# Performance work log

Measured on AMD Instinct MI355X. Metric: run time of the kernel, lower is better.

## Reference

```python
import jax, jax.numpy as jnp
import numpy as np

A_MIN = 0.001
EPS = 1e-08


def setup_inputs() -> dict:
    key = jax.random.key(0)
    k1, k2, k3, k4 = jax.random.split(key, 4)
    B, O, I = 512, 1024, 512
    x = jax.random.normal(k1, (B, I), dtype=jnp.float32)
    translation = jax.random.uniform(k2, (O, I), dtype=jnp.float32, minval=-1.0, maxval=1.0)
    scale_raw = jax.random.uniform(k3, (O, I), dtype=jnp.float32, minval=-2.0, maxval=0.0)
    weights = jax.random.normal(k4, (O, I), dtype=jnp.float32) * (1.0 / np.sqrt(I))
    return {"x": x, "translation": translation, "scale_raw": scale_raw, "weights": weights}


def reference(x, translation, scale_raw, weights):
    # x: (B, I); params: (O, I)
    scale = A_MIN + jax.nn.softplus(scale_raw)  # (O, I)
    # s: (B, O, I) broadcast intermediate
    s = (x[:, None, :] - translation[None, :, :]) / (scale[None, :, :] + EPS)
    s2 = s * s
    wavelet = (1.0 - s2) * jnp.exp(-0.5 * s2)  # mexican hat
    y = jnp.einsum('oi,boi->bo', weights, wavelet)  # reduce over in_features
    return y
```

## Files before the change

kernel.cpp:

```cpp
#include <hip/hip_runtime.h>
#include <hip/hip_bf16.h>


#define WL_A_MIN 0.001f
#define WL_EPS   1e-8f

constexpr int WL_B = 512;
constexpr int WL_O = 1024;
constexpr int WL_I = 512;

constexpr int O_TILE = 16;
constexpr int B_TILE = 64;
constexpr int KC     = 64;

constexpr int PS = KC * 4 + 4;
constexpr int XS = B_TILE + 4;

#define WL_SQK  0.84932180553704583800f
#define WL_IK   1.38629436111989061883f
#define WL_L2E  1.44269504088896340736f
#define WL_LN2  0.69314718055994530942f

typedef float v2f __attribute__((ext_vector_type(2)));

__device__ __forceinline__ float fast_exp2(float a) {
#if __has_builtin(__builtin_amdgcn_exp2f)
    return __builtin_amdgcn_exp2f(a);
#else
    return exp2f(a);
#endif
}
__device__ __forceinline__ float fast_log2(float a) {
#if __has_builtin(__builtin_amdgcn_logf)
    return __builtin_amdgcn_logf(a);
#else
    return __log2f(a);
#endif
}
__device__ __forceinline__ float fast_rcp(float a) {
#if __has_builtin(__builtin_amdgcn_rcpf)
    return __builtin_amdgcn_rcpf(a);
#else
    return 1.0f / a;
#endif
}

__global__ __launch_bounds__(256, 2) void wl_fused(
    const float* __restrict__ x,
    const float* __restrict__ translation,
    const float* __restrict__ scale_raw,
    const float* __restrict__ weights,
    float* __restrict__ out)
{
    __shared__ float p_lds[O_TILE * PS];
    __shared__ float x_lds[KC * XS];

    const int tid    = threadIdx.x;
    const int ox     = tid & 15;
    const int bg     = tid >> 4;
    const int o_base = blockIdx.x * O_TILE;
    const int b_base = blockIdx.y * B_TILE;

    v2f accA = {0.0f, 0.0f};
    v2f accB = {0.0f, 0.0f};

    for (int kc = 0; kc < WL_I; kc += KC) {
        #pragma unroll
        for (int k = 0; k < 4; ++k) {
            int lin = k * 256 + tid;
            int o_l = lin >> 6;
            int i_l = lin & 63;
            int gi  = (o_base + o_l) * WL_I + kc + i_l;
            float t  = translation[gi];
            float sr = scale_raw[gi];
            float w  = weights[gi];
            float ex    = fast_exp2(sr * WL_L2E);
            float sp    = fast_log2(1.0f + ex) * WL_LN2;
            float inv   = fast_rcp(WL_A_MIN + sp + WL_EPS);
            float inv_s = inv * WL_SQK;
            float4 pv = make_float4(-t * inv_s, inv_s, w, w * WL_IK);
            *reinterpret_cast<float4*>(&p_lds[o_l * PS + i_l * 4]) = pv;
        }
        {
            int b_r = tid & 63;
            int seg = tid >> 6;
            const float* xg = &x[(b_base + b_r) * WL_I + kc + seg * 16];
            #pragma unroll
            for (int q = 0; q < 4; ++q) {
                float4 v = *reinterpret_cast<const float4*>(&xg[q * 4]);
                int i0 = seg * 16 + q * 4;
                x_lds[(i0 + 0) * XS + b_r] = v.x;
                x_lds[(i0 + 1) * XS + b_r] = v.y;
                x_lds[(i0 + 2) * XS + b_r] = v.z;
                x_lds[(i0 + 3) * XS + b_r] = v.w;
            }
        }
        __syncthreads();

        const float* pr = &p_lds[ox * PS];

        #pragma unroll 4
        for (int i = 0; i < KC; ++i) {
            float4 p  = *reinterpret_cast<const float4*>(&pr[i * 4]);
            float4 xq = *reinterpret_cast<const float4*>(&x_lds[i * XS + bg * 4]);
            v2f nti2 = {p.x, p.x};
            v2f inv2 = {p.y, p.y};
            v2f w2   = {p.z, p.z};
            v2f nk2  = {-p.w, -p.w};
            v2f xa = {xq.x, xq.y};
            v2f xb = {xq.z, xq.w};
            v2f sa = __builtin_elementwise_fma(xa, inv2, nti2);
            v2f sb = __builtin_elementwise_fma(xb, inv2, nti2);
            v2f ua = sa * sa;
            v2f ub = sb * sb;
            v2f ea = {fast_exp2(-ua.x), fast_exp2(-ua.y)};
            v2f eb = {fast_exp2(-ub.x), fast_exp2(-ub.y)};
            accA = __builtin_elementwise_fma(w2, ea, accA);
            accB = __builtin_elementwise_fma(w2, eb, accB);
            v2f uea = ua * ea;
            v2f ueb = ub * eb;
            accA = __builtin_elementwise_fma(nk2, uea, accA);
            accB = __builtin_elementwise_fma(nk2, ueb, accB);
        }
        __syncthreads();
    }

    const int o = o_base + ox;
    const int b = b_base + bg * 4;
    out[(b + 0) * WL_O + o] = accA.x;
    out[(b + 1) * WL_O + o] = accA.y;
    out[(b + 2) * WL_O + o] = accB.x;
    out[(b + 3) * WL_O + o] = accB.y;
}

extern "C" void kernel_launch(void* const* d_in, const int* in_sizes, int n_in,
                              void* d_out, int out_size, void* d_ws, size_t ws_size,
                              hipStream_t stream) {
    const float* x           = (const float*)d_in[0];
    const float* translation = (const float*)d_in[1];
    const float* scale_raw   = (const float*)d_in[2];
    const float* weights     = (const float*)d_in[3];
    float*       out         = (float*)d_out;

    wl_fused<<<dim3(WL_O / O_TILE, WL_B / B_TILE), dim3(256), 0, stream>>>(
        x, translation, scale_raw, weights, out);
}
```

Measured before the change: 114.5 us.

## Split parameter preprocessing into separate kernel and stream transposed params from global

Adds a prep kernel that computes the softplus-derived per-(o,i) parameters once and writes them transposed as float4 into workspace. Previously every block in the batch dimension recomputed them. The main kernel stages a 32-row x tile for the full input dimension in LDS and reads the parameters straight from global memory, coalesced across lanes. Each thread now accumulates 8 batch rows instead of 4. This removes redundant transcendental work and the per-chunk syncs, but adds a second launch, an 8 MB workspace round-trip, and one-block-per-CU launch bounds that may reduce latency hiding.

Result: slower. 139.5 us (+21.8%).

```diff
diff --git a/kernel.cpp b/kernel.cpp
--- a/kernel.cpp
+++ b/kernel.cpp
@@ -8,13 +8,6 @@
 constexpr int WL_B = 512;
 constexpr int WL_O = 1024;
 constexpr int WL_I = 512;
-
-constexpr int O_TILE = 16;
-constexpr int B_TILE = 64;
-constexpr int KC     = 64;
-
-constexpr int PS = KC * 4 + 4;
-constexpr int XS = B_TILE + 4;
 
 #define WL_SQK  0.84932180553704583800f
 #define WL_IK   1.38629436111989061883f
@@ -45,92 +38,113 @@
 #endif
 }
 
-__global__ __launch_bounds__(256, 2) void wl_fused(
-    const float* __restrict__ x,
+__global__ __launch_bounds__(256) void wl_prep(
     const float* __restrict__ translation,
     const float* __restrict__ scale_raw,
     const float* __restrict__ weights,
+    float4* __restrict__ pT4)
+{
+    const int lane   = threadIdx.x & 63;
+    const int ic     = threadIdx.x >> 6;
+    const int o      = blockIdx.x * 64 + lane;
+    const int i_base = blockIdx.y * 64 + ic * 16;
+
+    #pragma unroll 4
+    for (int k = 0; k < 16; ++k) {
+        int i  = i_base + k;
+        int gi = o * WL_I + i;
+        float t  = translation[gi];
+        float sr = scale_raw[gi];
+        float w  = weights[gi];
+        float ex    = fast_exp2(sr * WL_L2E);
+        float sp    = fast_log2(1.0f + ex) * WL_LN2;
+        float inv   = fast_rcp(WL_A_MIN + sp + WL_EPS);
+        float inv_s = inv * WL_SQK;
+        pT4[i * WL_O + o] = make_float4(-t * inv_s, inv_s, w, w * WL_IK);
+    }
+}
+
+__global__ __launch_bounds__(256, 1) void wl_main(
+    const float* __restrict__ x,
+    const float4* __restrict__ pT4,
     float* __restrict__ out)
 {
-    __shared__ float p_lds[O_TILE * PS];
-    __shared__ float x_lds[KC * XS];
+    __shared__ float xT[WL_I * 32];
 
-    const int tid    = threadIdx.x;
-    const int ox     = tid & 15;
-    const int bg     = tid >> 4;
-    const int o_base = blockIdx.x * O_TILE;
-    const int b_base = blockIdx.y * B_TILE;
+    const int tid  = threadIdx.x;
+    const int lane = tid & 63;
+    const int wid  = __builtin_amdgcn_readfirstlane(tid >> 6);
+    const int o    = blockIdx.x * 64 + lane;
+    const int b0   = blockIdx.y * 32;
 
-    v2f accA = {0.0f, 0.0f};
-    v2f accB = {0.0f, 0.0f};
+    {
+        const int b_l = tid & 31;
+        const int seg = tid >> 5;
+        const float* xg = &x[(b0 + b_l) * WL_I + seg * 64];
+        #pragma unroll
+        for (int q = 0; q < 16; ++q) {
+            float4 v = *reinterpret_cast<const float4*>(xg + q * 4);
+            int i0 = seg * 64 + q * 4;
+            xT[(i0 + 0) * 32 + b_l] = v.x;
+            xT[(i0 + 1) * 32 + b_l] = v.y;
+            xT[(i0 + 2) * 32 + b_l] = v.z;
+            xT[(i0 + 3) * 32 + b_l] = v.w;
+        }
+    }
+    __syncthreads();
 
-    for (int kc = 0; kc < WL_I; kc += KC) {
-        #pragma unroll
-        for (int k = 0; k < 4; ++k) {
-            int lin = k * 256 + tid;
-            int o_l = lin >> 6;
-            int i_l = lin & 63;
-            int gi  = (o_base + o_l) * WL_I + kc + i_l;
-            float t  = translation[gi];
-            float sr = scale_raw[gi];
-            float w  = weights[gi];
-            float ex    = fast_exp2(sr * WL_L2E);
-            float sp    = fast_log2(1.0f + ex) * WL_LN2;
-            float inv   = fast_rcp(WL_A_MIN + sp + WL_EPS);
-            float inv_s = inv * WL_SQK;
-            float4 pv = make_float4(-t * inv_s, inv_s, w, w * WL_IK);
-            *reinterpret_cast<float4*>(&p_lds[o_l * PS + i_l * 4]) = pv;
-        }
-        {
-            int b_r = tid & 63;
-            int seg = tid >> 6;
-            const float* xg = &x[(b_base + b_r) * WL_I + kc + seg * 16];
-            #pragma unroll
-            for (int q = 0; q < 4; ++q) {
-                float4 v = *reinterpret_cast<const float4*>(&xg[q * 4]);
-                int i0 = seg * 16 + q * 4;
-                x_lds[(i0 + 0) * XS + b_r] = v.x;
-                x_lds[(i0 + 1) * XS + b_r] = v.y;
-                x_lds[(i0 + 2) * XS + b_r] = v.z;
-                x_lds[(i0 + 3) * XS + b_r] = v.w;
-            }
-        }
-        __syncthreads();
+    const float4* pp   = pT4 + o;
+    const float*  xrow = &xT[wid * 8];
 
-        const float* pr = &p_lds[ox * PS];
+    v2f a0 = {0.f, 0.f}, a1 = {0.f, 0.f}, a2 = {0.f, 0.f}, a3 = {0.f, 0.f};
 
-        #pragma unroll 4
-        for (int i = 0; i < KC; ++i) {
-            float4 p  = *reinterpret_cast<const float4*>(&pr[i * 4]);
-            float4 xq = *reinterpret_cast<const float4*>(&x_lds[i * XS + bg * 4]);
-            v2f nti2 = {p.x, p.x};
-            v2f inv2 = {p.y, p.y};
-            v2f w2   = {p.z, p.z};
-            v2f nk2  = {-p.w, -p.w};
-            v2f xa = {xq.x, xq.y};
-            v2f xb = {xq.z, xq.w};
-            v2f sa = __builtin_elementwise_fma(xa, inv2, nti2);
-            v2f sb = __builtin_elementwise_fma(xb, inv2, nti2);
-            v2f ua = sa * sa;
-            v2f ub = sb * sb;
-            v2f ea = {fast_exp2(-ua.x), fast_exp2(-ua.y)};
-            v2f eb = {fast_exp2(-ub.x), fast_exp2(-ub.y)};
-            accA = __builtin_elementwise_fma(w2, ea, accA);
-            accB = __builtin_elementwise_fma(w2, eb, accB);
-            v2f uea = ua * ea;
-            v2f ueb = ub * eb;
-            accA = __builtin_elementwise_fma(nk2, uea, accA);
-            accB = __builtin_elementwise_fma(nk2, ueb, accB);
-        }
-        __syncthreads();
+    #pragma unroll 4
+    for (int i = 0; i < WL_I; ++i) {
+        float4 p = pp[(size_t)i * WL_O];
+        float4 xa = *reinterpret_cast<const float4*>(xrow + i * 32);
+        float4 xb = *reinterpret_cast<const float4*>(xrow + i * 32 + 4);
+
+        v2f nti = {p.x, p.x};
+        v2f inv = {p.y, p.y};
+        v2f w2  = {p.z, p.z};
+        v2f wk  = {p.w, p.w};
+
+        v2f x01 = {xa.x, xa.y};
+        v2f x23 = {xa.z, xa.w};
+        v2f x45 = {xb.x, xb.y};
+        v2f x67 = {xb.z, xb.w};
+
+        v2f s0 = __builtin_elementwise_fma(x01, inv, nti);
+        v2f s1 = __builtin_elementwise_fma(x23, inv, nti);
+        v2f s2 = __builtin_elementwise_fma(x45, inv, nti);
+        v2f s3 = __builtin_elementwise_fma(x67, inv, nti);
+        v2f u0 = s0 * s0;
+        v2f u1 = s1 * s1;
+        v2f u2 = s2 * s2;
+        v2f u3 = s3 * s3;
+        v2f e0 = {fast_exp2(-u0.x), fast_exp2(-u0.y)};
+        v2f e1 = {fast_exp2(-u1.x), fast_exp2(-u1.y)};
+        v2f e2 = {fast_exp2(-u2.x), fast_exp2(-u2.y)};
+        v2f e3 = {fast_exp2(-u3.x), fast_exp2(-u3.y)};
+        a0 = __builtin_elementwise_fma(w2, e0, a0);
+        a1 = __builtin_elementwise_fma(w2, e1, a1);
+        a2 = __builtin_elementwise_fma(w2, e2, a2);
+        a3 = __builtin_elementwise_fma(w2, e3, a3);
+        a0 = __builtin_elementwise_fma(wk, -(u0 * e0), a0);
+        a1 = __builtin_elementwise_fma(wk, -(u1 * e1), a1);
+        a2 = __builtin_elementwise_fma(wk, -(u2 * e2), a2);
+        a3 = __builtin_elementwise_fma(wk, -(u3 * e3), a3);
     }
 
-    const int o = o_base + ox;
-    const int b = b_base + bg * 4;
-    out[(b + 0) * WL_O + o] = accA.x;
-    out[(b + 1) * WL_O + o] = accA.y;
-    out[(b + 2) * WL_O + o] = accB.x;
-    out[(b + 3) * WL_O + o] = accB.y;
+    const int b = b0 + wid * 8;
+    out[(b + 0) * WL_O + o] = a0.x;
+    out[(b + 1) * WL_O + o] = a0.y;
+    out[(b + 2) * WL_O + o] = a1.x;
+    out[(b + 3) * WL_O + o] = a1.y;
+    out[(b + 4) * WL_O + o] = a2.x;
+    out[(b + 5) * WL_O + o] = a2.y;
+    out[(b + 6) * WL_O + o] = a3.x;
+    out[(b + 7) * WL_O + o] = a3.y;
 }
 
 extern "C" void kernel_launch(void* const* d_in, const int* in_sizes, int n_in,
@@ -141,7 +155,11 @@
     const float* scale_raw   = (const float*)d_in[2];
     const float* weights     = (const float*)d_in[3];
     float*       out         = (float*)d_out;
+    float4*      pT4         = (float4*)d_ws;
 
-    wl_fused<<<dim3(WL_O / O_TILE, WL_B / B_TILE), dim3(256), 0, stream>>>(
-        x, translation, scale_raw, weights, out);
+    wl_prep<<<dim3(WL_O / 64, WL_I / 64), dim3(256), 0, stream>>>(
+        translation, scale_raw, weights, pT4);
+
+    wl_main<<<dim3(WL_O / 64, WL_B / 32), dim3(256), 0, stream>>>(
+        x, pT4, out);
 }
```
